# Kernel optimization log

Hardware: AMD Instinct MI355X
Metric: run time of the kernel (lower is better)

Reference implementation:

```python
import jax, jax.numpy as jnp
import numpy as np

N_BOXES = 2048
N_CLASSES = 20


def _cross(a, b):
    return a[..., 0] * b[..., 1] - a[..., 1] * b[..., 0]


def _corners(box):
    # box: [5] = cx, cy, w, h, angle -> [4,2] corner coords
    cx, cy, w, h, a = box[0], box[1], box[2], box[3], box[4]
    c, s = jnp.cos(a), jnp.sin(a)
    dx = jnp.array([-1.0, 1.0, 1.0, -1.0], box.dtype) * (w * 0.5)
    dy = jnp.array([-1.0, -1.0, 1.0, 1.0], box.dtype) * (h * 0.5)
    return jnp.stack([cx + c * dx - s * dy, cy + s * dx + c * dy], axis=-1)


def _points_in_box(pts, box):
    # pts [K,2]; rotate into box frame, test axis-aligned containment
    cx, cy, w, h, a = box[0], box[1], box[2], box[3], box[4]
    c, s = jnp.cos(a), jnp.sin(a)
    px = pts[:, 0] - cx
    py = pts[:, 1] - cy
    lx = c * px + s * py
    ly = -s * px + c * py
    eps = 1e-5
    return (jnp.abs(lx) <= w * 0.5 + eps) & (jnp.abs(ly) <= h * 0.5 + eps)


def _pair_inter_area(box_a, box_b):
    # Exact convex intersection area of two rotated rectangles.
    ca = _corners(box_a)
    cb = _corners(box_b)
    # all 4x4 edge-pair intersections
    p = ca[:, None, :]
    r = (jnp.roll(ca, -1, 0) - ca)[:, None, :]
    q = cb[None, :, :]
    s_ = (jnp.roll(cb, -1, 0) - cb)[None, :, :]
    denom = _cross(r, s_)
    qp = q - p
    safe = jnp.where(jnp.abs(denom) > 1e-9, denom, 1.0)
    t = _cross(qp, s_) / safe
    u = _cross(qp, r) / safe
    valid_e = (jnp.abs(denom) > 1e-9) & (t >= 0.0) & (t <= 1.0) & (u >= 0.0) & (u <= 1.0)
    ipts = p + t[..., None] * r  # [4,4,2]
    # candidate polygon vertices: corners of A in B, corners of B in A, edge crossings
    pts = jnp.concatenate([ca, cb, ipts.reshape(16, 2)], axis=0)  # [24,2]
    mask = jnp.concatenate([_points_in_box(ca, box_b), _points_in_box(cb, box_a), valid_e.reshape(16)], axis=0)
    k = jnp.sum(mask)
    m = mask.astype(pts.dtype)[:, None]
    center = jnp.sum(pts * m, axis=0) / jnp.maximum(k, 1).astype(pts.dtype)
    d = pts - center
    ang = jnp.where(mask, jnp.arctan2(d[:, 1], d[:, 0]), 1e9)  # invalid -> sorted last
    idx = jnp.argsort(ang)
    ds = d[idx]
    ar = jnp.arange(24)
    nxt = jnp.where(ar + 1 < k, ar + 1, 0)
    cr = _cross(ds, ds[nxt])
    area = 0.5 * jnp.abs(jnp.sum(jnp.where(ar < k, cr, 0.0)))
    return jnp.where(k >= 3, area, 0.0)


def _iou_one_vs_many(box, boxes):
    inter = jax.vmap(lambda b: _pair_inter_area(box, b))(boxes)  # [N]
    area_a = box[2] * box[3]
    area_b = boxes[:, 2] * boxes[:, 3]
    return inter / (area_a + area_b - inter + 1e-9)


def _rotated_nms_mask(boxes, scores, iou_threshold):
    # sequential greedy suppression, highest score first; returns bool keep mask (original order)
    n = boxes.shape[0]
    order = jnp.argsort(-scores)
    bs = boxes[order]
    ar = jnp.arange(n)

    def body(i, keep):
        ious = _iou_one_vs_many(bs[i], bs)
        suppress = (ious > iou_threshold) & (ar > i) & keep[i]
        return keep & ~suppress

    keep_sorted = jax.lax.fori_loop(0, n, body, jnp.ones((n,), bool))
    return jnp.zeros((n,), bool).at[order].set(keep_sorted)


def setup_inputs() -> dict:
    key = jax.random.key(0)
    k1, k2, k3, k4, k5 = jax.random.split(key, 5)
    cxcy = jax.random.uniform(k1, (N_BOXES, 2), jnp.float32) * 1024.0
    wh = jax.random.uniform(k2, (N_BOXES, 2), jnp.float32) * 96.0 + 4.0
    ang = jax.random.uniform(k3, (N_BOXES, 1), jnp.float32) * np.pi
    boxes = jnp.concatenate([cxcy, wh, ang], axis=1)  # [N,5]
    scores = jax.random.uniform(k4, (N_BOXES,), jnp.float32)
    labels = jax.random.randint(k5, (N_BOXES,), 0, N_CLASSES, dtype=jnp.int64 if jax.config.read('jax_enable_x64') else jnp.int32)
    return {"boxes": boxes, "scores": scores, "labels": labels, "iou_threshold": 0.5}


def reference(boxes, scores, labels, iou_threshold):
    # multiclass NMS via coordinate-offset trick (N <= 20000 branch of forward)
    cx, cy, w, h = boxes[:, 0], boxes[:, 1], boxes[:, 2], boxes[:, 3]
    max_radius = jnp.max(jnp.sqrt(w * w + h * h)) * 0.5
    max_coord = jnp.maximum(jnp.max(cx), jnp.max(cy))
    offset_scale = (max_coord + max_radius) * 2.0 + 1.0
    offsets = labels.astype(boxes.dtype) * offset_scale
    boxes_nms = boxes.at[:, 0].add(offsets).at[:, 1].add(offsets)
    keep = _rotated_nms_mask(boxes_nms, scores, iou_threshold)
    # fixed-shape encoding of the kept-index set: score of kept boxes, 0 for suppressed
    return scores * keep.astype(scores.dtype)
```

## Files before the change

kernel.cpp:

```cpp
#include <hip/hip_runtime.h>
#include <cstdint>

typedef unsigned long long u64;
typedef uint32_t u32;

#define NB 2048
#define EDGE_CAP 16384
#define CLIST_CAP 2048


__global__ __launch_bounds__(256) void build_kernel(
    const float* __restrict__ boxes, const float* __restrict__ scores,
    const int* __restrict__ labels,
    float* __restrict__ cxp, float* __restrict__ cyp, float* __restrict__ wp,
    float* __restrict__ hp, float* __restrict__ cp, float* __restrict__ sp,
    float4* __restrict__ pxyr, float* __restrict__ sscp, int* __restrict__ sidx,
    u32* __restrict__ counters) {
#pragma clang fp contract(off)
  __shared__ float sc[NB];
  __shared__ float smc[4], smr[4];
  int t = threadIdx.x;
  if (blockIdx.x == 0 && t < 4) counters[t] = 0u;
  float mc = -1e30f, mr = -1e30f;
  for (int k = t; k < NB; k += 256) {
    float cx = boxes[k * 5 + 0];
    float cy = boxes[k * 5 + 1];
    float w = boxes[k * 5 + 2];
    float h = boxes[k * 5 + 3];
    mc = fmaxf(mc, fmaxf(cx, cy));
    float ww = w * w;
    float hh = h * h;
    mr = fmaxf(mr, sqrtf(ww + hh));
    sc[k] = scores[k];
  }
  for (int off = 32; off > 0; off >>= 1) {
    mc = fmaxf(mc, __shfl_down(mc, off));
    mr = fmaxf(mr, __shfl_down(mr, off));
  }
  if ((t & 63) == 0) { smc[t >> 6] = mc; smr[t >> 6] = mr; }
  __syncthreads();
  mc = fmaxf(fmaxf(smc[0], smc[1]), fmaxf(smc[2], smc[3]));
  mr = fmaxf(fmaxf(smr[0], smr[1]), fmaxf(smr[2], smr[3]));
  float osc = (mc + mr * 0.5f) * 2.0f + 1.0f;

  int wave = t >> 6, lane = t & 63;
  int i = blockIdx.x * 4 + wave;
  float si = sc[i];
  int rank = 0;
#pragma unroll 8
  for (int m = 0; m < NB / 64; ++m) {
    int j = m * 64 + lane;
    float sj = sc[j];
    rank += (int)((sj > si) || (sj == si && j < i));
  }
  for (int off = 32; off > 0; off >>= 1) rank += __shfl_down(rank, off);
  if (lane == 0) {
    float off = (float)labels[i] * osc;
    float cx = boxes[i * 5 + 0] + off;
    float cy = boxes[i * 5 + 1] + off;
    float w = boxes[i * 5 + 2];
    float h = boxes[i * 5 + 3];
    float a = boxes[i * 5 + 4];
    float c = cosf(a);
    float s = sinf(a);
    float ww = w * w;
    float hh = h * h;
    float rad = 0.5f * sqrtf(ww + hh);
    cxp[rank] = cx;
    cyp[rank] = cy;
    wp[rank] = w;
    hp[rank] = h;
    cp[rank] = c;
    sp[rank] = s;
    pxyr[rank] = make_float4(cx, cy, rad, 0.0f);
    sscp[rank] = si;
    sidx[rank] = i;
  }
}

__global__ __launch_bounds__(256) void candgeom_greedy_kernel(
    const float* __restrict__ cxp, const float* __restrict__ cyp,
    const float* __restrict__ wp, const float* __restrict__ hp,
    const float* __restrict__ cp, const float* __restrict__ sp,
    const float4* __restrict__ pxyr, const float* __restrict__ thrp,
    const float* __restrict__ sscp, const int* __restrict__ sidx,
    u32* __restrict__ edges, u32* __restrict__ counters,
    float* __restrict__ out) {
#pragma clang fp contract(off)
  __shared__ u32 clist[CLIST_CAP];
  __shared__ float dxL[256 * 25];
  __shared__ float dyL[256 * 25];
  __shared__ u32 ccnt;
  __shared__ int is_last;
  __shared__ u64 keepw[32];
  __shared__ u32 Sw32[64];
  __shared__ int changed;
  int t = threadIdx.x;
  if (t == 0) ccnt = 0;
  float jx[8], jy[8], jr[8];
#pragma unroll
  for (int c = 0; c < 8; ++c) {
    float4 v = pxyr[c * 256 + t];
    jx[c] = v.x; jy[c] = v.y; jr[c] = v.z;
  }
  __syncthreads();
  int i0 = blockIdx.x * 4;
#pragma unroll
  for (int di = 0; di < 4; ++di) {
    int i = i0 + di;
    float4 pi = pxyr[i];
    float ax = pi.x, ay = pi.y, ar = pi.z;
#pragma unroll
    for (int c = 0; c < 8; ++c) {
      int j = c * 256 + t;
      if (j > i) {
        float dx = jx[c] - ax, dy = jy[c] - ay;
        float rr = ar + jr[c] + 1.0f;
        if (dx * dx + dy * dy <= rr * rr) {
          u32 s = atomicAdd(&ccnt, 1u);
          if (s < CLIST_CAP) clist[s] = ((u32)i << 16) | (u32)j;
        }
      }
    }
  }
  __syncthreads();
  u32 cnt = ccnt < CLIST_CAP ? ccnt : CLIST_CAP;
  float thr = *thrp;
  float* myDx = &dxL[t * 25];
  float* myDy = &dyL[t * 25];
  for (u32 idx = t; idx < cnt; idx += 256) {
    u32 pk = clist[idx];
    int bi = (int)(pk >> 16);
    int bj = (int)(pk & 0xFFFFu);
    float acx = cxp[bi], acy = cyp[bi], aw = wp[bi], ah = hp[bi];
    float ac = cp[bi], as_ = sp[bi];
    float bcx = cxp[bj], bcy = cyp[bj], bw = wp[bj], bh = hp[bj];
    float bc = cp[bj], bs_ = sp[bj];
    const float SX[4] = {-1.f, 1.f, 1.f, -1.f};
    const float SY[4] = {-1.f, -1.f, 1.f, 1.f};
    float axx[4], ayy[4], bxx[4], byy[4];
    float ahw = aw * 0.5f, ahh = ah * 0.5f;
    float bhw = bw * 0.5f, bhh = bh * 0.5f;
#pragma unroll
    for (int q = 0; q < 4; ++q) {
      float dx = SX[q] * ahw, dy = SY[q] * ahh;
      axx[q] = acx + ac * dx - as_ * dy;
      ayy[q] = acy + as_ * dx + ac * dy;
      float ex = SX[q] * bhw, ey = SY[q] * bhh;
      bxx[q] = bcx + bc * ex - bs_ * ey;
      byy[q] = bcy + bs_ * ex + bc * ey;
    }
    float px_[24], py_[24];
    bool mk[24];
#pragma unroll
    for (int q = 0; q < 4; ++q) {
      {
        float axp = axx[q] - bcx, ayp = ayy[q] - bcy;
        float lxx = bc * axp + bs_ * ayp;
        float lyy = bc * ayp - bs_ * axp;
        mk[q] = (fabsf(lxx) <= bhw + 1e-5f) && (fabsf(lyy) <= bhh + 1e-5f);
        px_[q] = axx[q]; py_[q] = ayy[q];
      }
      {
        float axp = bxx[q] - acx, ayp = byy[q] - acy;
        float lxx = ac * axp + as_ * ayp;
        float lyy = ac * ayp - as_ * axp;
        mk[4 + q] = (fabsf(lxx) <= ahw + 1e-5f) && (fabsf(lyy) <= ahh + 1e-5f);
        px_[4 + q] = bxx[q]; py_[4 + q] = byy[q];
      }
    }
#pragma unroll
    for (int e = 0; e < 4; ++e) {
      float rx = axx[(e + 1) & 3] - axx[e];
      float ry = ayy[(e + 1) & 3] - ayy[e];
#pragma unroll
      for (int f = 0; f < 4; ++f) {
        float sx = bxx[(f + 1) & 3] - bxx[f];
        float sy = byy[(f + 1) & 3] - byy[f];
        float denom = rx * sy - ry * sx;
        float qpx = bxx[f] - axx[e];
        float qpy = byy[f] - ayy[e];
        bool dn = fabsf(denom) > 1e-9f;
        float safe = dn ? denom : 1.0f;
        float tt = (qpx * sy - qpy * sx) / safe;
        float uu = (qpx * ry - qpy * rx) / safe;
        bool valid = dn && (tt >= 0.0f) && (tt <= 1.0f) && (uu >= 0.0f) && (uu <= 1.0f);
        int id = 8 + e * 4 + f;
        px_[id] = axx[e] + tt * rx;
        py_[id] = ayy[e] + tt * ry;
        mk[id] = valid;
      }
    }
    int k = 0;
    float sx0 = 0.0f, sy0 = 0.0f;
#pragma unroll
    for (int q = 0; q < 24; ++q) {
      if (mk[q]) { k++; sx0 += px_[q]; sy0 += py_[q]; }
    }
    float kkf = (float)(k > 0 ? k : 1);
    float cxm = sx0 / kkf, cym = sy0 / kkf;
    u64 key[32];
#pragma unroll
    for (int q = 0; q < 24; ++q) {
      float dx = px_[q] - cxm, dy = py_[q] - cym;
      myDx[q] = dx; myDy[q] = dy;
      float sm = fabsf(dx) + fabsf(dy);
      float r = (sm > 0.0f) ? dy / sm : 0.0f;
      float pa;
      if (dx >= 0.0f) pa = r;
      else pa = (__float_as_uint(dy) >> 31) ? (-2.0f - r) : (2.0f - r);
      float ang = mk[q] ? pa : 1e9f;
      u32 ub = __float_as_uint(ang);
      u32 v = (ub & 0x80000000u) ? ~ub : (ub | 0x80000000u);
      key[q] = (((u64)v) << 5) | (u64)q;
    }
#pragma unroll
    for (int q = 24; q < 32; ++q) key[q] = ~0ull;
#pragma unroll
    for (int kk2 = 2; kk2 <= 32; kk2 <<= 1) {
#pragma unroll
      for (int jj = kk2 >> 1; jj > 0; jj >>= 1) {
#pragma unroll
        for (int ii = 0; ii < 32; ++ii) {
          int ll = ii ^ jj;
          if (ll > ii) {
            bool up = ((ii & kk2) == 0);
            u64 ka = key[ii], kb = key[ll];
            bool sw = up ? (ka > kb) : (ka < kb);
            key[ii] = sw ? kb : ka;
            key[ll] = sw ? ka : kb;
          }
        }
      }
    }
    float acc = 0.0f;
    int id0 = (int)(key[0] & 31ull);
    float fx = myDx[id0], fy = myDy[id0];
    float curx = fx, cury = fy;
#pragma unroll
    for (int q = 0; q < 24; ++q) {
      if (q < k - 1) {
        int idn = (int)(key[q + 1] & 31ull);
        float nx = myDx[idn], ny = myDy[idn];
        acc += curx * ny - cury * nx;
        curx = nx; cury = ny;
      } else if (q == k - 1) {
        acc += curx * fy - cury * fx;
      }
    }
    float area = 0.5f * fabsf(acc);
    float inter = (k >= 3) ? area : 0.0f;
    float areaA = aw * ah;
    float areaB = bw * bh;
    float iou = inter / (areaA + areaB - inter + 1e-9f);
    if (iou > thr) {
      u32 e = atomicAdd(&counters[1], 1u);
      if (e < EDGE_CAP) edges[e] = pk;
    }
  }
  __syncthreads();
  if (t == 0) {
    __threadfence();
    u32 old = atomicAdd(&counters[2], 1u);
    is_last = (old == (u32)(gridDim.x - 1)) ? 1 : 0;
  }
  __syncthreads();
  if (!is_last) return;
  __threadfence();
  __syncthreads();
  u32 ecnt = counters[1];
  if (ecnt > EDGE_CAP) ecnt = EDGE_CAP;
  u32 nl = ecnt < CLIST_CAP ? ecnt : CLIST_CAP;
  for (u32 k = t; k < nl; k += 256) clist[k] = edges[k];
  if (t < 32) keepw[t] = ~0ull;
  __syncthreads();
  for (int iter = 0; iter < 2060; ++iter) {
    if (t < 64) Sw32[t] = 0u;
    if (t == 0) changed = 0;
    __syncthreads();
    for (u32 k = t; k < ecnt; k += 256) {
      u32 pk = (k < CLIST_CAP) ? clist[k] : edges[k];
      int i = (int)(pk >> 16);
      int j = (int)(pk & 0xFFFFu);
      if ((keepw[i >> 6] >> (i & 63)) & 1ull)
        atomicOr(&Sw32[j >> 5], 1u << (j & 31));
    }
    __syncthreads();
    if (t < 32) {
      u64 S = ((u64)Sw32[2 * t]) | (((u64)Sw32[2 * t + 1]) << 32);
      u64 nk = ~S;
      if (nk != keepw[t]) { keepw[t] = nk; changed = 1; }
    }
    __syncthreads();
    int ch = changed;
    __syncthreads();
    if (!ch) break;
  }
  for (int p = t; p < NB; p += 256) {
    int bit = (int)((keepw[p >> 6] >> (p & 63)) & 1ull);
    out[sidx[p]] = bit ? sscp[p] : 0.0f;
  }
}

extern "C" void kernel_launch(void* const* d_in, const int* in_sizes, int n_in,
                              void* d_out, int out_size, void* d_ws, size_t ws_size,
                              hipStream_t stream) {
  const float* boxes = (const float*)d_in[0];
  const float* scores = (const float*)d_in[1];
  const int* labels = (const int*)d_in[2];
  const float* thr = (const float*)d_in[3];
  float* out = (float*)d_out;

  char* base = (char*)d_ws;
  u32* counters = (u32*)base;
  float* arr = (float*)(base + 256);
  float* cxp = arr + 0 * NB;
  float* cyp = arr + 1 * NB;
  float* wp = arr + 2 * NB;
  float* hp = arr + 3 * NB;
  float* cp = arr + 4 * NB;
  float* sp = arr + 5 * NB;
  float* sscp = arr + 6 * NB;
  int* sidx = (int*)(base + 57600);
  float4* pxyr = (float4*)(base + 66048);
  u32* edges = (u32*)(base + 102400);

  build_kernel<<<512, 256, 0, stream>>>(boxes, scores, labels, cxp, cyp, wp, hp,
                                        cp, sp, pxyr, sscp, sidx, counters);
  candgeom_greedy_kernel<<<512, 256, 0, stream>>>(cxp, cyp, wp, hp, cp, sp,
                                                  pxyr, thr, sscp, sidx,
                                                  edges, counters, out);
}
```

Before: 88.42 us.

## Fuse build and candidate/greedy kernels into one cooperative kernel with grid barrier

Merges the sort/build kernel and the candidate-geometry/greedy kernel into a single cooperative launch of 256 blocks, each handling 8 boxes instead of 4. A software grid barrier (atomic counter plus spin with s_sleep) replaces the kernel boundary, and a tiny init kernel resets the counters. The aim is to remove one launch gap and the inter-kernel drain. The cost is halving the grid, which doubles per-block work, adds spin-wait overhead, and raises LDS pressure from the combined shared arrays.

```diff
diff --git a/kernel.cpp b/kernel.cpp
--- a/kernel.cpp
+++ b/kernel.cpp
@@ -7,20 +7,38 @@
 #define NB 2048
 #define EDGE_CAP 16384
 #define CLIST_CAP 2048
-
-
-__global__ __launch_bounds__(256) void build_kernel(
+#define NBLK 256
+
+
+__global__ __launch_bounds__(64) void init_kernel(u32* __restrict__ counters) {
+  if (threadIdx.x < 8) counters[threadIdx.x] = 0u;
+}
+
+__global__ __launch_bounds__(256) void nms_all_kernel(
     const float* __restrict__ boxes, const float* __restrict__ scores,
-    const int* __restrict__ labels,
+    const int* __restrict__ labels, const float* __restrict__ thrp,
     float* __restrict__ cxp, float* __restrict__ cyp, float* __restrict__ wp,
     float* __restrict__ hp, float* __restrict__ cp, float* __restrict__ sp,
     float4* __restrict__ pxyr, float* __restrict__ sscp, int* __restrict__ sidx,
-    u32* __restrict__ counters) {
+    u32* __restrict__ edges, u32* __restrict__ counters,
+    float* __restrict__ out) {
 #pragma clang fp contract(off)
   __shared__ float sc[NB];
   __shared__ float smc[4], smr[4];
+  __shared__ u32 clist[CLIST_CAP];
+  __shared__ float dxL[256 * 25];
+  __shared__ float dyL[256 * 25];
+  __shared__ u32 ccnt;
+  __shared__ int is_last;
+  __shared__ u64 keepw[32];
+  __shared__ u32 Sw32[64];
+  __shared__ int changed;
+
   int t = threadIdx.x;
-  if (blockIdx.x == 0 && t < 4) counters[t] = 0u;
+  int b = blockIdx.x;
+  int wave = t >> 6, lane = t & 63;
+
+  if (t == 0) ccnt = 0;
   float mc = -1e30f, mr = -1e30f;
   for (int k = t; k < NB; k += 256) {
     float cx = boxes[k * 5 + 0];
@@ -43,70 +61,63 @@
   mr = fmaxf(fmaxf(smr[0], smr[1]), fmaxf(smr[2], smr[3]));
   float osc = (mc + mr * 0.5f) * 2.0f + 1.0f;
 
-  int wave = t >> 6, lane = t & 63;
-  int i = blockIdx.x * 4 + wave;
-  float si = sc[i];
-  int rank = 0;
+#pragma unroll
+  for (int rep = 0; rep < 2; ++rep) {
+    int i = b * 8 + rep * 4 + wave;
+    float si = sc[i];
+    int rank = 0;
 #pragma unroll 8
-  for (int m = 0; m < NB / 64; ++m) {
-    int j = m * 64 + lane;
-    float sj = sc[j];
-    rank += (int)((sj > si) || (sj == si && j < i));
-  }
-  for (int off = 32; off > 0; off >>= 1) rank += __shfl_down(rank, off);
-  if (lane == 0) {
-    float off = (float)labels[i] * osc;
-    float cx = boxes[i * 5 + 0] + off;
-    float cy = boxes[i * 5 + 1] + off;
-    float w = boxes[i * 5 + 2];
-    float h = boxes[i * 5 + 3];
-    float a = boxes[i * 5 + 4];
-    float c = cosf(a);
-    float s = sinf(a);
-    float ww = w * w;
-    float hh = h * h;
-    float rad = 0.5f * sqrtf(ww + hh);
-    cxp[rank] = cx;
-    cyp[rank] = cy;
-    wp[rank] = w;
-    hp[rank] = h;
-    cp[rank] = c;
-    sp[rank] = s;
-    pxyr[rank] = make_float4(cx, cy, rad, 0.0f);
-    sscp[rank] = si;
-    sidx[rank] = i;
-  }
-}
-
-__global__ __launch_bounds__(256) void candgeom_greedy_kernel(
-    const float* __restrict__ cxp, const float* __restrict__ cyp,
-    const float* __restrict__ wp, const float* __restrict__ hp,
-    const float* __restrict__ cp, const float* __restrict__ sp,
-    const float4* __restrict__ pxyr, const float* __restrict__ thrp,
-    const float* __restrict__ sscp, const int* __restrict__ sidx,
-    u32* __restrict__ edges, u32* __restrict__ counters,
-    float* __restrict__ out) {
-#pragma clang fp contract(off)
-  __shared__ u32 clist[CLIST_CAP];
-  __shared__ float dxL[256 * 25];
-  __shared__ float dyL[256 * 25];
-  __shared__ u32 ccnt;
-  __shared__ int is_last;
-  __shared__ u64 keepw[32];
-  __shared__ u32 Sw32[64];
-  __shared__ int changed;
-  int t = threadIdx.x;
-  if (t == 0) ccnt = 0;
+    for (int m = 0; m < NB / 64; ++m) {
+      int j = m * 64 + lane;
+      float sj = sc[j];
+      rank += (int)((sj > si) || (sj == si && j < i));
+    }
+    for (int off = 32; off > 0; off >>= 1) rank += __shfl_down(rank, off);
+    if (lane == 0) {
+      float off = (float)labels[i] * osc;
+      float cx = boxes[i * 5 + 0] + off;
+      float cy = boxes[i * 5 + 1] + off;
+      float w = boxes[i * 5 + 2];
+      float h = boxes[i * 5 + 3];
+      float a = boxes[i * 5 + 4];
+      float c = cosf(a);
+      float s = sinf(a);
+      float ww = w * w;
+      float hh = h * h;
+      float rad = 0.5f * sqrtf(ww + hh);
+      cxp[rank] = cx;
+      cyp[rank] = cy;
+      wp[rank] = w;
+      hp[rank] = h;
+      cp[rank] = c;
+      sp[rank] = s;
+      pxyr[rank] = make_float4(cx, cy, rad, 0.0f);
+      sscp[rank] = si;
+      sidx[rank] = i;
+    }
+  }
+
+  __syncthreads();
+  if (t == 0) {
+    __threadfence();
+    atomicAdd(&counters[3], 1u);
+    while (__hip_atomic_load(&counters[3], __ATOMIC_RELAXED,
+                             __HIP_MEMORY_SCOPE_AGENT) < (u32)NBLK) {
+      __builtin_amdgcn_s_sleep(1);
+    }
+  }
+  __syncthreads();
+  __threadfence();
+
   float jx[8], jy[8], jr[8];
 #pragma unroll
   for (int c = 0; c < 8; ++c) {
     float4 v = pxyr[c * 256 + t];
     jx[c] = v.x; jy[c] = v.y; jr[c] = v.z;
   }
-  __syncthreads();
-  int i0 = blockIdx.x * 4;
-#pragma unroll
-  for (int di = 0; di < 4; ++di) {
+  int i0 = b * 8;
+#pragma unroll
+  for (int di = 0; di < 8; ++di) {
     int i = i0 + di;
     float4 pi = pxyr[i];
     float ax = pi.x, ay = pi.y, ar = pi.z;
@@ -262,7 +273,7 @@
   if (t == 0) {
     __threadfence();
     u32 old = atomicAdd(&counters[2], 1u);
-    is_last = (old == (u32)(gridDim.x - 1)) ? 1 : 0;
+    is_last = (old == (u32)(NBLK - 1)) ? 1 : 0;
   }
   __syncthreads();
   if (!is_last) return;
@@ -325,9 +336,11 @@
   float4* pxyr = (float4*)(base + 66048);
   u32* edges = (u32*)(base + 102400);
 
-  build_kernel<<<512, 256, 0, stream>>>(boxes, scores, labels, cxp, cyp, wp, hp,
-                                        cp, sp, pxyr, sscp, sidx, counters);
-  candgeom_greedy_kernel<<<512, 256, 0, stream>>>(cxp, cyp, wp, hp, cp, sp,
-                                                  pxyr, thr, sscp, sidx,
-                                                  edges, counters, out);
+  init_kernel<<<1, 64, 0, stream>>>(counters);
+  void* args[] = {(void*)&boxes, (void*)&scores, (void*)&labels, (void*)&thr,
+                  (void*)&cxp, (void*)&cyp, (void*)&wp, (void*)&hp,
+                  (void*)&cp, (void*)&sp, (void*)&pxyr, (void*)&sscp,
+                  (void*)&sidx, (void*)&edges, (void*)&counters, (void*)&out};
+  hipLaunchCooperativeKernel((const void*)nms_all_kernel, dim3(NBLK), dim3(256),
+                             args, 0, stream);
 }
```

After: 137.9 us. 56.0% more time.
